# Kernel tuning notes

Measured on AMD Instinct MI355X. Metric: run time of the kernel, lower is better.

The kernel has to match this reference:

```python
import jax, jax.numpy as jnp
import numpy as np

B, S, D, H = 2, 2048, 1024, 16
DH = D // H  # 64


def setup_inputs() -> dict:
    key = jax.random.key(0)
    ks = jax.random.split(key, 12)
    inp = {
        "hidden_states": jax.random.normal(ks[0], (B, S, D), dtype=jnp.float32),
        "attention_mask": jax.random.randint(ks[1], (B, S), 0, 2, dtype=jnp.int32),
        "Wq": jax.random.normal(ks[2], (D, D), dtype=jnp.float32) / np.sqrt(D),
        "bq": jnp.zeros((D,), dtype=jnp.float32),
        "Wk": jax.random.normal(ks[3], (D, D), dtype=jnp.float32) / np.sqrt(D),
        "bk": jnp.zeros((D,), dtype=jnp.float32),
        "Wv": jax.random.normal(ks[4], (D, D), dtype=jnp.float32) / np.sqrt(D),
        "bv": jnp.zeros((D,), dtype=jnp.float32),
        # per-head additive query bias (emotion manipulation path)
        "emotion_w": jax.random.normal(ks[5], (H, DH), dtype=jnp.float32),
        "Wo": jax.random.normal(ks[6], (D, D), dtype=jnp.float32) / np.sqrt(D),
        "bo": jnp.zeros((D,), dtype=jnp.float32),
    }
    return inp


def reference(hidden_states, attention_mask, Wq, bq, Wk, bk, Wv, bv, emotion_w, Wo, bo):
    b, s, d = hidden_states.shape
    # projections -> [b, h, s, dh]
    def proj(W, bias):
        y = hidden_states @ W + bias
        return y.reshape(b, s, H, DH).transpose(0, 2, 1, 3)

    q = proj(Wq, bq)
    k = proj(Wk, bk)
    v = proj(Wv, bv)

    # manipulation_type='emotion': additive per-head query bias
    q = q + emotion_w[None, :, None, :]

    scores = jnp.einsum("bhqd,bhkd->bhqk", q, k) / np.sqrt(DH).astype(np.float32)
    # key-padding mask: positions where mask==0 get -inf
    scores = jnp.where(attention_mask[:, None, None, :] == 0, -jnp.inf, scores)
    attn = jax.nn.softmax(scores, axis=-1)  # dropout is identity in eval mode

    out = jnp.einsum("bhqk,bhkd->bhqd", attn, v)
    out = out.transpose(0, 2, 1, 3).reshape(b, s, d)
    return out @ Wo + bo
```

## Files before the change

### kernel.cpp

```cpp
#include <hip/hip_runtime.h>
#include <hip/hip_bf16.h>


#define B_  2
#define S_  2048
#define D_  1024
#define K_  1024
#define H_  16
#define DH_ 64
#define BS_ (B_*S_)

typedef __hip_bfloat16 bf16;
typedef __attribute__((ext_vector_type(8))) short s8v;
typedef __attribute__((ext_vector_type(4))) short s4v;
typedef __attribute__((ext_vector_type(4))) float f4v;
typedef __attribute__((ext_vector_type(16))) float f16v;

__device__ __forceinline__ float b2f(bf16 x) { return __bfloat162float(x); }
__device__ __forceinline__ bf16  f2b(float x) { return __float2bfloat16(x); }

__device__ __forceinline__ void gl_lds_16B(const bf16* g, bf16* l) {
    __builtin_amdgcn_global_load_lds(
        (const __attribute__((address_space(1))) unsigned int*)g,
        (__attribute__((address_space(3))) unsigned int*)l, 16, 0, 0);
}

__device__ __forceinline__ unsigned cvtpk_bf16(float a, float b) {
    unsigned r;
    asm("v_cvt_pk_bf16_f32 %0, %1, %2" : "=v"(r) : "v"(a), "v"(b));
    return r;
}
__device__ __forceinline__ void plswap(unsigned &a, unsigned &b) {
    asm("v_permlane32_swap_b32 %0, %1" : "+v"(a), "+v"(b));
}

#define QSCALE_ 0.1803368801f

__global__ __launch_bounds__(256) void prep_kernel(
    const float* __restrict__ X, const int* __restrict__ mask,
    const float* __restrict__ Wq, const float* __restrict__ Wk,
    const float* __restrict__ Wv, const float* __restrict__ Wo,
    bf16* __restrict__ Xb, bf16* __restrict__ mkbf,
    bf16* __restrict__ WTq, bf16* __restrict__ WTk,
    bf16* __restrict__ WTv, bf16* __restrict__ WTo)
{
    __shared__ float Ls[64][68];
    const int blk = blockIdx.x;
    const int t   = threadIdx.x;

    if (blk < 1024) {
        const int z   = blk >> 8;
        const int t16 = blk & 255;
        const int k0  = (t16 >> 4) * 64;
        const int n0  = (t16 & 15) * 64;
        const float* __restrict__ W = (z == 0) ? Wq : (z == 1) ? Wk : (z == 2) ? Wv : Wo;
        bf16* __restrict__ WT       = (z == 0) ? WTq : (z == 1) ? WTk : (z == 2) ? WTv : WTo;

        const int lr = t >> 4;
        const int lc = (t & 15) * 4;
        #pragma unroll
        for (int i = 0; i < 4; i++) {
            const int k = i * 16 + lr;
            const float4 v = *(const float4*)(W + (size_t)(k0 + k) * K_ + n0 + lc);
            Ls[k][lc + 0] = v.x; Ls[k][lc + 1] = v.y;
            Ls[k][lc + 2] = v.z; Ls[k][lc + 3] = v.w;
        }
        __syncthreads();
        #pragma unroll
        for (int i = 0; i < 4; i++) {
            const int n = i * 16 + lr;
            s4v o;
            #pragma unroll
            for (int j = 0; j < 4; j++) {
                bf16 tb = f2b(Ls[lc + j][n]);
                o[j] = *(short*)&tb;
            }
            *(s4v*)(WT + (size_t)(n0 + n) * K_ + k0 + lc) = o;
        }
    } else if (blk < 5120) {
        const size_t idx = ((size_t)(blk - 1024) * 256 + t) * 4;
        const float4 v = *(const float4*)(X + idx);
        bf16 t0 = f2b(v.x), t1 = f2b(v.y), t2 = f2b(v.z), t3 = f2b(v.w);
        s4v o;
        o[0] = *(short*)&t0; o[1] = *(short*)&t1;
        o[2] = *(short*)&t2; o[3] = *(short*)&t3;
        *(s4v*)(Xb + idx) = o;
    } else {
        const int idx = (blk - 5120) * 256 + t;
        mkbf[idx] = f2b(mask[idx] ? 1.0f : 0.0f);
    }
}

template <bool SWAPPED>
__device__ __forceinline__ void gemm_tile(
    const bf16* __restrict__ A, const bf16* __restrict__ BT,
    int m0, int n0, bf16* As, bf16* Bs, f4v acc[4][4])
{
    const int t    = threadIdx.x;
    const int lane = t & 63;
    const int wave = t >> 6;
    const int quad = lane >> 4;
    const int l15  = lane & 15;
    const int wr   = wave >> 1;
    const int wc   = wave & 1;

    const int sr = t >> 3;
    const int sc = (t & 7) * 8;

    for (int kb = 0; kb < K_; kb += 64) {
        #pragma unroll
        for (int i = 0; i < 4; i++) {
            const int r = i * 32 + sr;
            gl_lds_16B(A  + (size_t)(m0 + r) * K_ + kb + sc, As + r * 64 + sc);
            gl_lds_16B(BT + (size_t)(n0 + r) * K_ + kb + sc, Bs + r * 64 + sc);
        }
        __syncthreads();

        #pragma unroll
        for (int ks = 0; ks < 2; ks++) {
            s8v fA[4], fB[4];
            #pragma unroll
            for (int i = 0; i < 4; i++) {
                fA[i] = *(const s8v*)&As[(wr * 64 + i * 16 + l15) * 64 + ks * 32 + quad * 8];
                fB[i] = *(const s8v*)&Bs[(wc * 64 + i * 16 + l15) * 64 + ks * 32 + quad * 8];
            }
            #pragma unroll
            for (int i = 0; i < 4; i++)
                #pragma unroll
                for (int j = 0; j < 4; j++)
                    acc[i][j] = SWAPPED
                        ? __builtin_amdgcn_mfma_f32_16x16x32_bf16(fB[i], fA[j], acc[i][j], 0, 0, 0)
                        : __builtin_amdgcn_mfma_f32_16x16x32_bf16(fA[i], fB[j], acc[i][j], 0, 0, 0);
        }
        __syncthreads();
    }
}

__global__ __launch_bounds__(256) void proj_qkv_kernel(
    const bf16* __restrict__ Xb,
    const bf16* __restrict__ WTq, const float* __restrict__ bq,
    const bf16* __restrict__ WTk, const float* __restrict__ bk,
    const bf16* __restrict__ WTv, const float* __restrict__ bv,
    const float* __restrict__ emo, const int* __restrict__ mask,
    bf16* __restrict__ q_ws, bf16* __restrict__ k_ws, bf16* __restrict__ v_ws)
{
    const int m0 = blockIdx.x * 128;
    const int n0 = blockIdx.y * 128;
    const int z  = blockIdx.z;

    __shared__ __align__(16) bf16 As[128 * 64];
    __shared__ __align__(16) bf16 Bs[128 * 64];

    const int t    = threadIdx.x;
    const int lane = t & 63;
    const int wave = t >> 6;
    const int quad = lane >> 4;
    const int l15  = lane & 15;
    const int wr   = wave >> 1;
    const int wc   = wave & 1;

    f4v acc[4][4] = {};

    if (z == 0) {
        gemm_tile<false>(Xb, WTq, m0, n0, As, Bs, acc);
        #pragma unroll
        for (int j = 0; j < 4; j++) {
            const int n  = n0 + wc * 64 + j * 16 + l15;
            const int h  = n >> 6, dh = n & 63;
            const float bias_n = bq[n] + emo[n];
            #pragma unroll
            for (int i = 0; i < 4; i++) {
                #pragma unroll
                for (int r = 0; r < 4; r++) {
                    const int m = m0 + wr * 64 + i * 16 + quad * 4 + r;
                    const int b = m >> 11, s = m & 2047;
                    q_ws[(((size_t)(b * H_ + h)) * S_ + s) * DH_ + dh] =
                        f2b((acc[i][j][r] + bias_n) * QSCALE_);
                }
            }
        }
    } else if (z == 1) {
        gemm_tile<false>(Xb, WTk, m0, n0, As, Bs, acc);
        #pragma unroll
        for (int j = 0; j < 4; j++) {
            const int n  = n0 + wc * 64 + j * 16 + l15;
            const int h  = n >> 6, dh = n & 63;
            const float bias_n = bk[n];
            #pragma unroll
            for (int i = 0; i < 4; i++) {
                #pragma unroll
                for (int r = 0; r < 4; r++) {
                    const int m = m0 + wr * 64 + i * 16 + quad * 4 + r;
                    const int b = m >> 11, s = m & 2047;
                    k_ws[(((size_t)(b * H_ + h)) * S_ + s) * DH_ + dh] =
                        f2b(acc[i][j][r] + bias_n);
                }
            }
        }
    } else {
        gemm_tile<true>(Xb, WTv, m0, n0, As, Bs, acc);
        #pragma unroll
        for (int j = 0; j < 4; j++) {
            const int m = m0 + wr * 64 + j * 16 + l15;
            const int b = m >> 11, s = m & 2047;
            const float msk = mask[b * S_ + s] ? 1.0f : 0.0f;
            #pragma unroll
            for (int i = 0; i < 4; i++) {
                #pragma unroll
                for (int r = 0; r < 4; r++) {
                    const int n  = n0 + wc * 64 + i * 16 + quad * 4 + r;
                    const int h  = n >> 6, dh = n & 63;
                    v_ws[(((size_t)(b * H_ + h)) * DH_ + dh) * S_ + s] =
                        f2b((acc[i][j][r] + bv[n]) * msk);
                }
            }
        }
    }
}

__global__ __launch_bounds__(256) void proj_out_kernel(
    const bf16* __restrict__ ctx, const bf16* __restrict__ WTo,
    const float* __restrict__ bo, float* __restrict__ out)
{
    const int m0 = blockIdx.x * 128;
    const int n0 = blockIdx.y * 128;

    __shared__ __align__(16) bf16 As[128 * 64];
    __shared__ __align__(16) bf16 Bs[128 * 64];

    const int t    = threadIdx.x;
    const int lane = t & 63;
    const int wave = t >> 6;
    const int quad = lane >> 4;
    const int l15  = lane & 15;
    const int wr   = wave >> 1;
    const int wc   = wave & 1;

    f4v acc[4][4] = {};
    gemm_tile<false>(ctx, WTo, m0, n0, As, Bs, acc);

    #pragma unroll
    for (int j = 0; j < 4; j++) {
        const int n = n0 + wc * 64 + j * 16 + l15;
        const float bias_n = bo[n];
        #pragma unroll
        for (int i = 0; i < 4; i++) {
            #pragma unroll
            for (int r = 0; r < 4; r++) {
                const int m = m0 + wr * 64 + i * 16 + quad * 4 + r;
                out[(size_t)m * D_ + n] = acc[i][j][r] + bias_n;
            }
        }
    }
}

__global__ __launch_bounds__(256) void attn_kernel(
    const bf16* __restrict__ q_ws, const bf16* __restrict__ k_ws,
    const bf16* __restrict__ v_ws, const bf16* __restrict__ mkbf,
    bf16* __restrict__ ctx)
{
    const int bh = blockIdx.x;
    const int q0 = blockIdx.y * 128;
    const int b  = bh >> 4;
    const int h  = bh & 15;

    __shared__ __align__(16) bf16 k_lds[2][64 * 64];
    __shared__ __align__(16) bf16 vt_lds[2][64 * 64];

    const int t    = threadIdx.x;
    const int wave = t >> 6;
    const int lane = t & 63;
    const int ql   = lane & 31;
    const int hf   = lane >> 5;
    const int swz  = ql & 7;

    s8v qf[4];
    #pragma unroll
    for (int kd = 0; kd < 4; kd++)
        qf[kd] = *(const s8v*)(q_ws +
            ((size_t)bh * S_ + q0 + wave * 32 + ql) * DH_ + kd * 16 + hf * 8);

    f16v oacc[2] = {};
    f16v osum    = {};

    const bf16* __restrict__ mbase = mkbf + (size_t)b * S_;

    int srw[2], scs[2];
    #pragma unroll
    for (int c = 0; c < 2; c++) {
        const int e = c * 2048 + t * 8;
        srw[c] = e >> 6;
        scs[c] = ((e >> 3) & 7) ^ (srw[c] & 7);
    }

    auto stage = [&](int kb0, bf16* kd_, bf16* vd_) {
        #pragma unroll
        for (int c = 0; c < 2; c++) {
            const int e = c * 2048 + t * 8;
            const int r = srw[c], cs = scs[c];
            gl_lds_16B(k_ws + ((size_t)bh * S_ + kb0 + r) * DH_ + cs * 8,
                       kd_ + e);
            gl_lds_16B(v_ws + ((size_t)bh * DH_ + r) * S_ + kb0 + cs * 8,
                       vd_ + e);
        }
    };

    stage(0, k_lds[0], vt_lds[0]);
    __syncthreads();

    int cur = 0;
    for (int kb0 = 0; kb0 < S_; kb0 += 64) {
        if (kb0 + 64 < S_)
            stage(kb0 + 64, k_lds[cur ^ 1], vt_lds[cur ^ 1]);

        const bf16* __restrict__ kc = k_lds[cur];
        const bf16* __restrict__ vc = vt_lds[cur];

        f16v sacc[2] = {};
        __builtin_amdgcn_s_setprio(1);
        #pragma unroll
        for (int kt = 0; kt < 2; kt++) {
            #pragma unroll
            for (int kd = 0; kd < 4; kd++) {
                const s8v kf = *(const s8v*)&kc[(kt * 32 + ql) * 64 +
                                                ((kd * 2 + hf) ^ swz) * 8];
                sacc[kt] = __builtin_amdgcn_mfma_f32_32x32x16_bf16(kf, qf[kd], sacc[kt], 0, 0, 0);
            }
        }
        __builtin_amdgcn_s_setprio(0);

        #pragma unroll
        for (int kt = 0; kt < 2; kt++) {
            #pragma unroll
            for (int hh = 0; hh < 2; hh++) {
                const int ks = kt * 2 + hh;
                float p[8];
                #pragma unroll
                for (int j = 0; j < 8; j++)
                    p[j] = exp2f(sacc[kt][hh * 8 + j]);
                unsigned w0 = cvtpk_bf16(p[0], p[1]);
                unsigned w1 = cvtpk_bf16(p[2], p[3]);
                unsigned w2 = cvtpk_bf16(p[4], p[5]);
                unsigned w3 = cvtpk_bf16(p[6], p[7]);
                plswap(w0, w2);
                plswap(w1, w3);
                union { unsigned u[4]; s8v v; } af;
                af.u[0] = w0; af.u[1] = w1; af.u[2] = w2; af.u[3] = w3;

                const s8v mf = *(const s8v*)(mbase + kb0 + ks * 16 + hf * 8);
                __builtin_amdgcn_s_setprio(1);
                osum = __builtin_amdgcn_mfma_f32_32x32x16_bf16(af.v, mf, osum, 0, 0, 0);
                #pragma unroll
                for (int dt = 0; dt < 2; dt++) {
                    const s8v vf = *(const s8v*)&vc[(dt * 32 + ql) * 64 +
                                                    ((ks * 2 + hf) ^ swz) * 8];
                    oacc[dt] = __builtin_amdgcn_mfma_f32_32x32x16_bf16(af.v, vf, oacc[dt], 0, 0, 0);
                }
                __builtin_amdgcn_s_setprio(0);
            }
        }

        __syncthreads();
        cur ^= 1;
    }

    #pragma unroll
    for (int r = 0; r < 16; r++) {
        const float inv = 1.0f / osum[r];
        const int q = q0 + wave * 32 + (r & 3) + 8 * (r >> 2) + 4 * hf;
        #pragma unroll
        for (int dt = 0; dt < 2; dt++)
            ctx[((size_t)b * S_ + q) * D_ + h * DH_ + dt * 32 + ql] =
                f2b(oacc[dt][r] * inv);
    }
}

extern "C" void kernel_launch(void* const* d_in, const int* in_sizes, int n_in,
                              void* d_out, int out_size, void* d_ws, size_t ws_size,
                              hipStream_t stream) {
    (void)in_sizes; (void)n_in; (void)out_size; (void)ws_size;

    const float* X    = (const float*)d_in[0];
    const int*   mask = (const int*)d_in[1];
    const float* Wq   = (const float*)d_in[2];
    const float* bq   = (const float*)d_in[3];
    const float* Wk   = (const float*)d_in[4];
    const float* bk   = (const float*)d_in[5];
    const float* Wv   = (const float*)d_in[6];
    const float* bv   = (const float*)d_in[7];
    const float* emo  = (const float*)d_in[8];
    const float* Wo   = (const float*)d_in[9];
    const float* bo   = (const float*)d_in[10];
    float* out = (float*)d_out;

    bf16* q_ws = (bf16*)d_ws;
    bf16* k_ws = q_ws + (size_t)BS_ * D_;
    bf16* v_ws = k_ws + (size_t)BS_ * D_;
    bf16* ctx  = v_ws + (size_t)BS_ * D_;
    bf16* Xb   = ctx  + (size_t)BS_ * D_;
    bf16* WTq  = Xb   + (size_t)BS_ * D_;
    bf16* WTk  = WTq  + (size_t)D_ * K_;
    bf16* WTv  = WTk  + (size_t)D_ * K_;
    bf16* WTo  = WTv  + (size_t)D_ * K_;
    bf16* mkbf = WTo  + (size_t)D_ * K_;

    hipLaunchKernelGGL(prep_kernel, dim3(5136), dim3(256), 0, stream,
                       X, mask, Wq, Wk, Wv, Wo, Xb, mkbf, WTq, WTk, WTv, WTo);
    hipLaunchKernelGGL(proj_qkv_kernel, dim3(BS_ / 128, D_ / 128, 3), dim3(256), 0, stream,
                       Xb, WTq, bq, WTk, bk, WTv, bv, emo, mask, q_ws, k_ws, v_ws);
    hipLaunchKernelGGL(attn_kernel, dim3(B_ * H_, S_ / 128), dim3(256), 0, stream,
                       q_ws, k_ws, v_ws, mkbf, ctx);
    hipLaunchKernelGGL(proj_out_kernel, dim3(BS_ / 128, D_ / 128), dim3(256), 0, stream,
                       ctx, WTo, bo, out);
}
```

Before: 234.2 us.

## Split attention key range across two wave groups and merge partial sums in LDS

The attention block grows from 256 to 512 threads. Two groups of four waves each process half of the key sequence for the same 128 queries, with separate double-buffered LDS staging. At the end, group 1 writes its unnormalized output and row sums to LDS and group 0 adds them before normalizing. This is meant to halve the serial key loop per block and add latency hiding, at the cost of more LDS, a merge step, and possibly fewer resident blocks per CU. The merge relies on the softmax not subtracting a running max, so the partial results can simply be added.

```diff
diff --git a/kernel.cpp b/kernel.cpp
--- a/kernel.cpp
+++ b/kernel.cpp
@@ -254,7 +254,7 @@
     }
 }
 
-__global__ __launch_bounds__(256) void attn_kernel(
+__global__ __launch_bounds__(512) void attn_kernel(
     const bf16* __restrict__ q_ws, const bf16* __restrict__ k_ws,
     const bf16* __restrict__ v_ws, const bf16* __restrict__ mkbf,
     bf16* __restrict__ ctx)
@@ -264,21 +264,25 @@
     const int b  = bh >> 4;
     const int h  = bh & 15;
 
-    __shared__ __align__(16) bf16 k_lds[2][64 * 64];
-    __shared__ __align__(16) bf16 vt_lds[2][64 * 64];
+    __shared__ __align__(16) bf16 lds[2][2][2][4096];
 
     const int t    = threadIdx.x;
     const int wave = t >> 6;
+    const int qsub = wave & 3;
+    const int grp  = wave >> 2;
+    const int tg   = t & 255;
     const int lane = t & 63;
     const int ql   = lane & 31;
     const int hf   = lane >> 5;
     const int swz  = ql & 7;
 
+    const int kb_base = grp * 1024;
+
     s8v qf[4];
     #pragma unroll
     for (int kd = 0; kd < 4; kd++)
         qf[kd] = *(const s8v*)(q_ws +
-            ((size_t)bh * S_ + q0 + wave * 32 + ql) * DH_ + kd * 16 + hf * 8);
+            ((size_t)bh * S_ + q0 + qsub * 32 + ql) * DH_ + kd * 16 + hf * 8);
 
     f16v oacc[2] = {};
     f16v osum    = {};
@@ -288,33 +292,33 @@
     int srw[2], scs[2];
     #pragma unroll
     for (int c = 0; c < 2; c++) {
-        const int e = c * 2048 + t * 8;
+        const int e = c * 2048 + tg * 8;
         srw[c] = e >> 6;
         scs[c] = ((e >> 3) & 7) ^ (srw[c] & 7);
     }
 
-    auto stage = [&](int kb0, bf16* kd_, bf16* vd_) {
+    auto stage = [&](int kb_abs, int buf) {
         #pragma unroll
         for (int c = 0; c < 2; c++) {
-            const int e = c * 2048 + t * 8;
+            const int e = c * 2048 + tg * 8;
             const int r = srw[c], cs = scs[c];
-            gl_lds_16B(k_ws + ((size_t)bh * S_ + kb0 + r) * DH_ + cs * 8,
-                       kd_ + e);
-            gl_lds_16B(v_ws + ((size_t)bh * DH_ + r) * S_ + kb0 + cs * 8,
-                       vd_ + e);
+            gl_lds_16B(k_ws + ((size_t)bh * S_ + kb_abs + r) * DH_ + cs * 8,
+                       &lds[grp][buf][0][e]);
+            gl_lds_16B(v_ws + ((size_t)bh * DH_ + r) * S_ + kb_abs + cs * 8,
+                       &lds[grp][buf][1][e]);
         }
     };
 
-    stage(0, k_lds[0], vt_lds[0]);
+    stage(kb_base, 0);
     __syncthreads();
 
     int cur = 0;
-    for (int kb0 = 0; kb0 < S_; kb0 += 64) {
-        if (kb0 + 64 < S_)
-            stage(kb0 + 64, k_lds[cur ^ 1], vt_lds[cur ^ 1]);
-
-        const bf16* __restrict__ kc = k_lds[cur];
-        const bf16* __restrict__ vc = vt_lds[cur];
+    for (int kb = 0; kb < 1024; kb += 64) {
+        if (kb + 64 < 1024)
+            stage(kb_base + kb + 64, cur ^ 1);
+
+        const bf16* __restrict__ kc = &lds[grp][cur][0][0];
+        const bf16* __restrict__ vc = &lds[grp][cur][1][0];
 
         f16v sacc[2] = {};
         __builtin_amdgcn_s_setprio(1);
@@ -347,7 +351,7 @@
                 union { unsigned u[4]; s8v v; } af;
                 af.u[0] = w0; af.u[1] = w1; af.u[2] = w2; af.u[3] = w3;
 
-                const s8v mf = *(const s8v*)(mbase + kb0 + ks * 16 + hf * 8);
+                const s8v mf = *(const s8v*)(mbase + kb_base + kb + ks * 16 + hf * 8);
                 __builtin_amdgcn_s_setprio(1);
                 osum = __builtin_amdgcn_mfma_f32_32x32x16_bf16(af.v, mf, osum, 0, 0, 0);
                 #pragma unroll
@@ -364,14 +368,33 @@
         cur ^= 1;
     }
 
-    #pragma unroll
-    for (int r = 0; r < 16; r++) {
-        const float inv = 1.0f / osum[r];
-        const int q = q0 + wave * 32 + (r & 3) + 8 * (r >> 2) + 4 * hf;
-        #pragma unroll
-        for (int dt = 0; dt < 2; dt++)
-            ctx[((size_t)b * S_ + q) * D_ + h * DH_ + dt * 32 + ql] =
-                f2b(oacc[dt][r] * inv);
+    float* mg = (float*)&lds[0][0][0][0];
+
+    if (grp == 1) {
+        #pragma unroll
+        for (int r = 0; r < 16; r++) {
+            const int qrow = (r & 3) + 8 * (r >> 2) + 4 * hf;
+            #pragma unroll
+            for (int dt = 0; dt < 2; dt++)
+                mg[qsub * 2048 + qrow * 64 + dt * 32 + ql] = oacc[dt][r];
+            if (ql == 0)
+                mg[8192 + qsub * 32 + qrow] = osum[r];
+        }
+    }
+    __syncthreads();
+    if (grp == 0) {
+        #pragma unroll
+        for (int r = 0; r < 16; r++) {
+            const int qrow = (r & 3) + 8 * (r >> 2) + 4 * hf;
+            const float den = osum[r] + mg[8192 + qsub * 32 + qrow];
+            const float inv = 1.0f / den;
+            const int q = q0 + qsub * 32 + qrow;
+            #pragma unroll
+            for (int dt = 0; dt < 2; dt++) {
+                const float o = oacc[dt][r] + mg[qsub * 2048 + qrow * 64 + dt * 32 + ql];
+                ctx[((size_t)b * S_ + q) * D_ + h * DH_ + dt * 32 + ql] = f2b(o * inv);
+            }
+        }
     }
 }
 
@@ -408,7 +431,7 @@
                        X, mask, Wq, Wk, Wv, Wo, Xb, mkbf, WTq, WTk, WTv, WTo);
     hipLaunchKernelGGL(proj_qkv_kernel, dim3(BS_ / 128, D_ / 128, 3), dim3(256), 0, stream,
                        Xb, WTq, bq, WTk, bk, WTv, bv, emo, mask, q_ws, k_ws, v_ws);
-    hipLaunchKernelGGL(attn_kernel, dim3(B_ * H_, S_ / 128), dim3(256), 0, stream,
+    hipLaunchKernelGGL(attn_kernel, dim3(B_ * H_, S_ / 128), dim3(512), 0, stream,
                        q_ws, k_ws, v_ws, mkbf, ctx);
     hipLaunchKernelGGL(proj_out_kernel, dim3(BS_ / 128, D_ / 128), dim3(256), 0, stream,
                        ctx, WTo, bo, out);
```

New measurement: 227.9 us. -2.7%, faster.
